# Optimization experiments

Hardware: AMD Instinct MI355X
Metric: run time of the kernel (lower is better)

The kernel has to match this reference:

```python
import jax, jax.numpy as jnp
import numpy as np


def _cdist_p2(x, y):
    # x: [N, t1, h], y: [N, t2, h] -> [N, t1, t2] Euclidean distances
    x2 = jnp.sum(x * x, axis=-1)  # [N, t1]
    y2 = jnp.sum(y * y, axis=-1)  # [N, t2]
    xy = jnp.einsum('nik,njk->nij', x, y)  # [N, t1, t2]
    d2 = x2[:, :, None] + y2[None if False else slice(None), None, :] - 2.0 * xy
    d2 = jnp.maximum(d2, 0.0)
    return jnp.sqrt(d2)


def _solve_relaxed_wmd(scores, axis):
    # argmin + one-hot scatter + (mask*scores).mean() == sum of per-slice minima / scores.size
    idx = jnp.argmin(scores, axis=axis, keepdims=True)
    mins = jnp.take_along_axis(scores, idx, axis=axis)
    return jnp.sum(mins) / scores.size


def setup_inputs() -> dict:
    key = jax.random.key(0)
    kx, ky = jax.random.split(key)
    L, B, t1, t2, h = 4, 16, 1024, 1024, 128
    x = jax.random.normal(kx, (L, B, t1, h), dtype=jnp.float32)
    y = jax.random.normal(ky, (L, B, t2, h), dtype=jnp.float32)
    return {"x": x, "y": y}


def reference(x, y):
    L, B, t1, h = x.shape
    t2 = y.shape[2]
    xf = x.reshape(L * B, t1, h).astype(jnp.float32)
    yf = y.reshape(L * B, t2, h).astype(jnp.float32)
    scores = _cdist_p2(xf, yf)  # [L*B, t1, t2]
    forward_scores = _solve_relaxed_wmd(scores, axis=1)
    backward_scores = _solve_relaxed_wmd(scores, axis=2)
    return jnp.maximum(forward_scores, backward_scores)
```

## Files before the change

### kernel.cpp

```cpp
#include <hip/hip_runtime.h>

#define NB 64
#define T 1024
#define HD 128

#define EINF 0xFF800000u

typedef __attribute__((ext_vector_type(8))) short bf16x8;
typedef __attribute__((ext_vector_type(4))) float f32x4;

static __device__ __forceinline__ short f2bf(float f) {
    unsigned u = __float_as_uint(f);
    u += 0x7FFFu + ((u >> 16) & 1u);
    return (short)(u >> 16);
}

static __device__ __forceinline__ unsigned fenc(float f) {
    unsigned b = __float_as_uint(f);
    return b ^ (unsigned)(((int)b >> 31) | (int)0x80000000);
}
static __device__ __forceinline__ float fdec(unsigned u) {
    unsigned m = (~(unsigned)((int)u >> 31)) | 0x80000000u;
    return __uint_as_float(u ^ m);
}

__global__ void wmd_init(unsigned* __restrict__ g_colmin, float* __restrict__ sums) {
    int t = blockIdx.x * 256 + threadIdx.x;
    if (t < NB * T) g_colmin[t] = EINF;
    if (t < 2) sums[t] = 0.f;
}

__global__ void wmd_convy(const float* __restrict__ y, short* __restrict__ ybf,
                          float* __restrict__ y2) {
    int idx = blockIdx.x * 256 + threadIdx.x;
    float4 v = reinterpret_cast<const float4*>(y)[idx];
    short4 s4;
    s4.x = f2bf(v.x); s4.y = f2bf(v.y); s4.z = f2bf(v.z); s4.w = f2bf(v.w);
    reinterpret_cast<short4*>(ybf)[idx] = s4;
    float p = v.x * v.x + v.y * v.y + v.z * v.z + v.w * v.w;
    p += __shfl_xor(p, 1);  p += __shfl_xor(p, 2);  p += __shfl_xor(p, 4);
    p += __shfl_xor(p, 8);  p += __shfl_xor(p, 16);
    if ((threadIdx.x & 31) == 0) y2[idx >> 5] = p;
}

__global__ __launch_bounds__(256, 2)
void wmd_main(const float* __restrict__ x, const short* __restrict__ ybf,
              const float* __restrict__ y2, unsigned* __restrict__ g_colmin,
              float* __restrict__ g_rowmin) {
    __shared__ short b_sm[2][128 * 128];
    __shared__ float x2_sm[128];
    __shared__ unsigned col_min_sm[1024];
    __shared__ unsigned row_min_sm[128];

    const int tid  = threadIdx.x;
    const int n    = blockIdx.y;
    const int i0   = blockIdx.x * 128;
    const int lane = tid & 63;
    const int wave = tid >> 6;
    const int wm   = wave >> 1, wn = wave & 1;
    const int l16  = lane & 15, quad = lane >> 4;
    const float FINF = __uint_as_float(0x7F800000u);

    #pragma unroll
    for (int e = tid; e < 1024; e += 256) col_min_sm[e] = EINF;
    if (tid < 128) row_min_sm[tid] = EINF;

    {
        const float4* xg = reinterpret_cast<const float4*>(x + (size_t)(n * T + i0) * HD);
        #pragma unroll
        for (int it = 0; it < 16; ++it) {
            int idx = it * 256 + tid;
            int row = idx >> 5, c4 = idx & 31;
            float4 v = xg[idx];
            short4 s4;
            s4.x = f2bf(v.x); s4.y = f2bf(v.y); s4.z = f2bf(v.z); s4.w = f2bf(v.w);
            int c  = c4 >> 1;
            int sw = c ^ (row & 7);
            *reinterpret_cast<short4*>(&b_sm[0][(row * 16 + sw) * 8 + (c4 & 1) * 4]) = s4;
            float p = v.x * v.x + v.y * v.y + v.z * v.z + v.w * v.w;
            p += __shfl_xor(p, 1);  p += __shfl_xor(p, 2);  p += __shfl_xor(p, 4);
            p += __shfl_xor(p, 8);  p += __shfl_xor(p, 16);
            if ((tid & 31) == 0) x2_sm[row] = p;
        }
    }
    __syncthreads();

    bf16x8 af[4][4];
    #pragma unroll
    for (int mi = 0; mi < 4; ++mi)
        #pragma unroll
        for (int kk = 0; kk < 4; ++kk) {
            int row = wm * 64 + mi * 16 + l16;
            int c   = kk * 4 + quad;
            af[mi][kk] = *reinterpret_cast<const bf16x8*>(
                &b_sm[0][(row * 16 + (c ^ (row & 7))) * 8]);
        }
    float x2v[16];
    #pragma unroll
    for (int mi = 0; mi < 4; ++mi)
        #pragma unroll
        for (int r = 0; r < 4; ++r)
            x2v[mi * 4 + r] = x2_sm[wm * 64 + mi * 16 + quad * 4 + r];
    float rmin[16];
    #pragma unroll
    for (int q = 0; q < 16; ++q) rmin[q] = FINF;

#define ISSUE_GLLS(pbuf, jtile)                                                   \
    {                                                                             \
        const short* ybase = ybf + (((size_t)(n * T + (jtile) * 128)) << 7);      \
        _Pragma("unroll")                                                         \
        for (int it = 0; it < 8; ++it) {                                          \
            int g   = wave * 8 + it;                                              \
            int s   = g * 64 + lane;                                              \
            int row = s >> 4;                                                     \
            int c   = (s & 15) ^ (row & 7);                                       \
            const short* gp = ybase + row * 128 + c * 8;                          \
            __builtin_amdgcn_global_load_lds(                                     \
                (const __attribute__((address_space(1))) void*)gp,                \
                (__attribute__((address_space(3))) void*)&b_sm[pbuf][g * 512],    \
                16, 0, 0);                                                        \
        }                                                                         \
    }

    ISSUE_GLLS(1, 0);

    for (int jt = 0; jt < 8; ++jt) {
        const int p = (jt & 1) ^ 1;
        __syncthreads();
        if (jt < 7) ISSUE_GLLS(p ^ 1, jt + 1);

        float y2v[4];
        #pragma unroll
        for (int ni = 0; ni < 4; ++ni)
            y2v[ni] = y2[n * T + jt * 128 + wn * 64 + ni * 16 + l16];

        f32x4 acc[4][4];
        #pragma unroll
        for (int mi = 0; mi < 4; ++mi)
            #pragma unroll
            for (int ni = 0; ni < 4; ++ni) {
                f32x4 z = {0.f, 0.f, 0.f, 0.f};
                acc[mi][ni] = z;
            }

        #pragma unroll
        for (int kk = 0; kk < 4; ++kk) {
            bf16x8 bv[4];
            #pragma unroll
            for (int ni = 0; ni < 4; ++ni) {
                int row = wn * 64 + ni * 16 + l16;
                int c   = kk * 4 + quad;
                bv[ni] = *reinterpret_cast<const bf16x8*>(
                    &b_sm[p][(row * 16 + (c ^ (row & 7))) * 8]);
            }
            #pragma unroll
            for (int mi = 0; mi < 4; ++mi)
                #pragma unroll
                for (int ni = 0; ni < 4; ++ni)
                    acc[mi][ni] = __builtin_amdgcn_mfma_f32_16x16x32_bf16(
                        af[mi][kk], bv[ni], acc[mi][ni], 0, 0, 0);
        }

        float vcol[4] = {FINF, FINF, FINF, FINF};
        #pragma unroll
        for (int mi = 0; mi < 4; ++mi)
            #pragma unroll
            for (int r = 0; r < 4; ++r) {
                float x2r = x2v[mi * 4 + r];
                #pragma unroll
                for (int ni = 0; ni < 4; ++ni) {
                    float xy = acc[mi][ni][r];
                    rmin[mi * 4 + r] = fminf(rmin[mi * 4 + r], fmaf(-2.f, xy, y2v[ni]));
                    vcol[ni]         = fminf(vcol[ni],         fmaf(-2.f, xy, x2r));
                }
            }
        #pragma unroll
        for (int ni = 0; ni < 4; ++ni) {
            float v = vcol[ni];
            v = fminf(v, __shfl_xor(v, 16));
            v = fminf(v, __shfl_xor(v, 32));
            if (lane < 16)
                atomicMin(&col_min_sm[jt * 128 + wn * 64 + ni * 16 + lane], fenc(v));
        }
    }

    #pragma unroll
    for (int mi = 0; mi < 4; ++mi)
        #pragma unroll
        for (int r = 0; r < 4; ++r) {
            float v = rmin[mi * 4 + r];
            v = fminf(v, __shfl_xor(v, 1));
            v = fminf(v, __shfl_xor(v, 2));
            v = fminf(v, __shfl_xor(v, 4));
            v = fminf(v, __shfl_xor(v, 8));
            if (l16 == 0)
                atomicMin(&row_min_sm[wm * 64 + mi * 16 + quad * 4 + r], fenc(v));
        }
    __syncthreads();
    if (tid < 128) {
        float rv = fdec(row_min_sm[tid]) + x2_sm[tid];
        g_rowmin[n * T + i0 + tid] = fmaxf(rv, 0.f);
    }
    #pragma unroll
    for (int e = tid; e < 1024; e += 256)
        atomicMin(&g_colmin[n * T + e], col_min_sm[e]);
}

__global__ void wmd_reduce(const unsigned* __restrict__ g_colmin,
                           const float* __restrict__ g_rowmin,
                           const float* __restrict__ y2,
                           float* __restrict__ sums) {
    int n = blockIdx.x, t = threadIdx.x;
    float sc = 0.f, sr = 0.f;
    for (int e = t; e < T; e += 256) {
        float cv = fdec(g_colmin[n * T + e]) + y2[n * T + e];
        sc += sqrtf(fmaxf(cv, 0.f));
        sr += sqrtf(g_rowmin[n * T + e]);
    }
    #pragma unroll
    for (int o = 1; o < 64; o <<= 1) {
        sc += __shfl_xor(sc, o);
        sr += __shfl_xor(sr, o);
    }
    __shared__ float bc[4], br[4];
    int lane = t & 63, wv = t >> 6;
    if (lane == 0) { bc[wv] = sc; br[wv] = sr; }
    __syncthreads();
    if (t == 0) {
        atomicAdd(&sums[0], bc[0] + bc[1] + bc[2] + bc[3]);
        atomicAdd(&sums[1], br[0] + br[1] + br[2] + br[3]);
    }
}

__global__ void wmd_finalize(const float* __restrict__ sums, float* __restrict__ out) {
    out[0] = fmaxf(sums[0], sums[1]) * (1.0f / 67108864.0f);
}

extern "C" void kernel_launch(void* const* d_in, const int* in_sizes, int n_in,
                              void* d_out, int out_size, void* d_ws, size_t ws_size,
                              hipStream_t stream) {
    const float* x = (const float*)d_in[0];
    const float* y = (const float*)d_in[1];
    float* out = (float*)d_out;

    char* ws = (char*)d_ws;
    unsigned* g_colmin = (unsigned*)(ws);
    float*    g_rowmin = (float*)(ws + 256 * 1024);
    float*    y2       = (float*)(ws + 512 * 1024);
    float*    sums     = (float*)(ws + 768 * 1024);
    short*    ybf      = (short*)(ws + 1024 * 1024);

    wmd_init<<<(NB * T + 255) / 256, 256, 0, stream>>>(g_colmin, sums);
    wmd_convy<<<(NB * T * HD / 4) / 256, 256, 0, stream>>>(y, ybf, y2);
    wmd_main<<<dim3(T / 128, NB), 256, 0, stream>>>(x, ybf, y2, g_colmin, g_rowmin);
    wmd_reduce<<<NB, 256, 0, stream>>>(g_colmin, g_rowmin, y2, sums);
    wmd_finalize<<<1, 1, 0, stream>>>(sums, out);
}
```

Before: 136.1 us.

## Split column range across blocks, shrink tiles, fuse init kernels and finalize

The main kernel now splits each batch's j range into two halves of 512, so the grid doubles to 16x64 blocks. Each block uses 64-row B tiles and one 32-row A slab per wave, which lowers LDS and register use enough to allow 4 blocks per CU. Row minima go to global memory through atomicMin, and x2 is written out so the reduce kernel can finish the row sums. Init is merged into the y-conversion kernel, and the finalize kernel is replaced by a last-block counter inside reduce, which removes two launches. In exchange, each x tile is loaded twice and there is more global atomic traffic.

```diff
diff --git a/kernel.cpp b/kernel.cpp
--- a/kernel.cpp
+++ b/kernel.cpp
@@ -14,7 +14,6 @@
     u += 0x7FFFu + ((u >> 16) & 1u);
     return (short)(u >> 16);
 }
-
 static __device__ __forceinline__ unsigned fenc(float f) {
     unsigned b = __float_as_uint(f);
     return b ^ (unsigned)(((int)b >> 31) | (int)0x80000000);
@@ -24,93 +23,52 @@
     return __uint_as_float(u ^ m);
 }
 
-__global__ void wmd_init(unsigned* __restrict__ g_colmin, float* __restrict__ sums) {
-    int t = blockIdx.x * 256 + threadIdx.x;
-    if (t < NB * T) g_colmin[t] = EINF;
-    if (t < 2) sums[t] = 0.f;
-}
-
-__global__ void wmd_convy(const float* __restrict__ y, short* __restrict__ ybf,
-                          float* __restrict__ y2) {
-    int idx = blockIdx.x * 256 + threadIdx.x;
-    float4 v = reinterpret_cast<const float4*>(y)[idx];
+__global__ void wmd_prep(const float* __restrict__ y, short* __restrict__ ybf,
+                         float* __restrict__ y2, unsigned* __restrict__ g_colmin,
+                         unsigned* __restrict__ g_rowmin, float* __restrict__ sums,
+                         unsigned* __restrict__ counter) {
+    int gi = blockIdx.x * 256 + threadIdx.x;
+    float4 v = reinterpret_cast<const float4*>(y)[gi];
     short4 s4;
     s4.x = f2bf(v.x); s4.y = f2bf(v.y); s4.z = f2bf(v.z); s4.w = f2bf(v.w);
-    reinterpret_cast<short4*>(ybf)[idx] = s4;
+    reinterpret_cast<short4*>(ybf)[gi] = s4;
     float p = v.x * v.x + v.y * v.y + v.z * v.z + v.w * v.w;
     p += __shfl_xor(p, 1);  p += __shfl_xor(p, 2);  p += __shfl_xor(p, 4);
     p += __shfl_xor(p, 8);  p += __shfl_xor(p, 16);
-    if ((threadIdx.x & 31) == 0) y2[idx >> 5] = p;
-}
-
-__global__ __launch_bounds__(256, 2)
+    if ((threadIdx.x & 31) == 0) y2[gi >> 5] = p;
+    if (gi < NB * T) { g_colmin[gi] = EINF; g_rowmin[gi] = EINF; }
+    if (gi < 2) sums[gi] = 0.f;
+    if (gi == 2) counter[0] = 0u;
+}
+
+__global__ __launch_bounds__(256, 4)
 void wmd_main(const float* __restrict__ x, const short* __restrict__ ybf,
-              const float* __restrict__ y2, unsigned* __restrict__ g_colmin,
-              float* __restrict__ g_rowmin) {
-    __shared__ short b_sm[2][128 * 128];
+              const float* __restrict__ y2g, unsigned* __restrict__ g_colmin,
+              unsigned* __restrict__ g_rowmin, float* __restrict__ x2g) {
+    __shared__ short b_sm[2][64 * 128];
+    __shared__ float y2_sm[512];
     __shared__ float x2_sm[128];
-    __shared__ unsigned col_min_sm[1024];
-    __shared__ unsigned row_min_sm[128];
+    __shared__ unsigned col_min_sm[512];
 
     const int tid  = threadIdx.x;
     const int n    = blockIdx.y;
-    const int i0   = blockIdx.x * 128;
+    const int bx   = blockIdx.x;
+    const int i0   = (bx & 7) * 128;
+    const int j0   = (bx >> 3) * 512;
     const int lane = tid & 63;
     const int wave = tid >> 6;
-    const int wm   = wave >> 1, wn = wave & 1;
     const int l16  = lane & 15, quad = lane >> 4;
     const float FINF = __uint_as_float(0x7F800000u);
 
     #pragma unroll
-    for (int e = tid; e < 1024; e += 256) col_min_sm[e] = EINF;
-    if (tid < 128) row_min_sm[tid] = EINF;
-
-    {
-        const float4* xg = reinterpret_cast<const float4*>(x + (size_t)(n * T + i0) * HD);
-        #pragma unroll
-        for (int it = 0; it < 16; ++it) {
-            int idx = it * 256 + tid;
-            int row = idx >> 5, c4 = idx & 31;
-            float4 v = xg[idx];
-            short4 s4;
-            s4.x = f2bf(v.x); s4.y = f2bf(v.y); s4.z = f2bf(v.z); s4.w = f2bf(v.w);
-            int c  = c4 >> 1;
-            int sw = c ^ (row & 7);
-            *reinterpret_cast<short4*>(&b_sm[0][(row * 16 + sw) * 8 + (c4 & 1) * 4]) = s4;
-            float p = v.x * v.x + v.y * v.y + v.z * v.z + v.w * v.w;
-            p += __shfl_xor(p, 1);  p += __shfl_xor(p, 2);  p += __shfl_xor(p, 4);
-            p += __shfl_xor(p, 8);  p += __shfl_xor(p, 16);
-            if ((tid & 31) == 0) x2_sm[row] = p;
-        }
-    }
-    __syncthreads();
-
-    bf16x8 af[4][4];
-    #pragma unroll
-    for (int mi = 0; mi < 4; ++mi)
-        #pragma unroll
-        for (int kk = 0; kk < 4; ++kk) {
-            int row = wm * 64 + mi * 16 + l16;
-            int c   = kk * 4 + quad;
-            af[mi][kk] = *reinterpret_cast<const bf16x8*>(
-                &b_sm[0][(row * 16 + (c ^ (row & 7))) * 8]);
-        }
-    float x2v[16];
-    #pragma unroll
-    for (int mi = 0; mi < 4; ++mi)
-        #pragma unroll
-        for (int r = 0; r < 4; ++r)
-            x2v[mi * 4 + r] = x2_sm[wm * 64 + mi * 16 + quad * 4 + r];
-    float rmin[16];
-    #pragma unroll
-    for (int q = 0; q < 16; ++q) rmin[q] = FINF;
+    for (int e = tid; e < 512; e += 256) col_min_sm[e] = EINF;
 
 #define ISSUE_GLLS(pbuf, jtile)                                                   \
     {                                                                             \
-        const short* ybase = ybf + (((size_t)(n * T + (jtile) * 128)) << 7);      \
+        const short* ybase = ybf + (((size_t)(n * T + j0 + (jtile) * 64)) << 7);  \
         _Pragma("unroll")                                                         \
-        for (int it = 0; it < 8; ++it) {                                          \
-            int g   = wave * 8 + it;                                              \
+        for (int it = 0; it < 4; ++it) {                                          \
+            int g   = wave * 4 + it;                                              \
             int s   = g * 64 + lane;                                              \
             int row = s >> 4;                                                     \
             int c   = (s & 15) ^ (row & 7);                                       \
@@ -122,21 +80,59 @@
         }                                                                         \
     }
 
-    ISSUE_GLLS(1, 0);
+    ISSUE_GLLS(0, 0);
+
+    bf16x8 af[2][4];
+    #pragma unroll
+    for (int mi = 0; mi < 2; ++mi) {
+        float part = 0.f;
+        #pragma unroll
+        for (int kk = 0; kk < 4; ++kk) {
+            const float4* gp = reinterpret_cast<const float4*>(
+                x + (((size_t)(n * T + i0 + wave * 32 + mi * 16 + l16)) << 7) + kk * 32 + quad * 8);
+            float4 a = gp[0], b = gp[1];
+            bf16x8 f;
+            f[0] = f2bf(a.x); f[1] = f2bf(a.y); f[2] = f2bf(a.z); f[3] = f2bf(a.w);
+            f[4] = f2bf(b.x); f[5] = f2bf(b.y); f[6] = f2bf(b.z); f[7] = f2bf(b.w);
+            af[mi][kk] = f;
+            part += a.x * a.x + a.y * a.y + a.z * a.z + a.w * a.w;
+            part += b.x * b.x + b.y * b.y + b.z * b.z + b.w * b.w;
+        }
+        part += __shfl_xor(part, 16);
+        part += __shfl_xor(part, 32);
+        if (quad == 0) {
+            x2_sm[wave * 32 + mi * 16 + l16] = part;
+            x2g[n * T + i0 + wave * 32 + mi * 16 + l16] = part;
+        }
+    }
+    #pragma unroll
+    for (int e = tid; e < 512; e += 256) y2_sm[e] = y2g[n * T + j0 + e];
+
+    float rmin[8];
+    #pragma unroll
+    for (int q = 0; q < 8; ++q) rmin[q] = FINF;
+
+    __syncthreads();
+
+    float x2v[8];
+    #pragma unroll
+    for (int mi = 0; mi < 2; ++mi)
+        #pragma unroll
+        for (int r = 0; r < 4; ++r)
+            x2v[mi * 4 + r] = x2_sm[wave * 32 + mi * 16 + quad * 4 + r];
 
     for (int jt = 0; jt < 8; ++jt) {
-        const int p = (jt & 1) ^ 1;
-        __syncthreads();
+        const int p = jt & 1;
         if (jt < 7) ISSUE_GLLS(p ^ 1, jt + 1);
 
         float y2v[4];
         #pragma unroll
         for (int ni = 0; ni < 4; ++ni)
-            y2v[ni] = y2[n * T + jt * 128 + wn * 64 + ni * 16 + l16];
-
-        f32x4 acc[4][4];
-        #pragma unroll
-        for (int mi = 0; mi < 4; ++mi)
+            y2v[ni] = y2_sm[jt * 64 + ni * 16 + l16];
+
+        f32x4 acc[2][4];
+        #pragma unroll
+        for (int mi = 0; mi < 2; ++mi)
             #pragma unroll
             for (int ni = 0; ni < 4; ++ni) {
                 f32x4 z = {0.f, 0.f, 0.f, 0.f};
@@ -148,13 +144,12 @@
             bf16x8 bv[4];
             #pragma unroll
             for (int ni = 0; ni < 4; ++ni) {
-                int row = wn * 64 + ni * 16 + l16;
-                int c   = kk * 4 + quad;
-                bv[ni] = *reinterpret_cast<const bf16x8*>(
-                    &b_sm[p][(row * 16 + (c ^ (row & 7))) * 8]);
+                int row = ni * 16 + l16;
+                int c   = (kk * 4 + quad) ^ (row & 7);
+                bv[ni] = *reinterpret_cast<const bf16x8*>(&b_sm[p][(row * 16 + c) * 8]);
             }
             #pragma unroll
-            for (int mi = 0; mi < 4; ++mi)
+            for (int mi = 0; mi < 2; ++mi)
                 #pragma unroll
                 for (int ni = 0; ni < 4; ++ni)
                     acc[mi][ni] = __builtin_amdgcn_mfma_f32_16x16x32_bf16(
@@ -163,7 +158,7 @@
 
         float vcol[4] = {FINF, FINF, FINF, FINF};
         #pragma unroll
-        for (int mi = 0; mi < 4; ++mi)
+        for (int mi = 0; mi < 2; ++mi)
             #pragma unroll
             for (int r = 0; r < 4; ++r) {
                 float x2r = x2v[mi * 4 + r];
@@ -180,12 +175,13 @@
             v = fminf(v, __shfl_xor(v, 16));
             v = fminf(v, __shfl_xor(v, 32));
             if (lane < 16)
-                atomicMin(&col_min_sm[jt * 128 + wn * 64 + ni * 16 + lane], fenc(v));
-        }
-    }
-
-    #pragma unroll
-    for (int mi = 0; mi < 4; ++mi)
+                atomicMin(&col_min_sm[jt * 64 + ni * 16 + lane], fenc(v));
+        }
+        __syncthreads();
+    }
+
+    #pragma unroll
+    for (int mi = 0; mi < 2; ++mi)
         #pragma unroll
         for (int r = 0; r < 4; ++r) {
             float v = rmin[mi * 4 + r];
@@ -194,28 +190,27 @@
             v = fminf(v, __shfl_xor(v, 4));
             v = fminf(v, __shfl_xor(v, 8));
             if (l16 == 0)
-                atomicMin(&row_min_sm[wm * 64 + mi * 16 + quad * 4 + r], fenc(v));
-        }
-    __syncthreads();
-    if (tid < 128) {
-        float rv = fdec(row_min_sm[tid]) + x2_sm[tid];
-        g_rowmin[n * T + i0 + tid] = fmaxf(rv, 0.f);
-    }
-    #pragma unroll
-    for (int e = tid; e < 1024; e += 256)
-        atomicMin(&g_colmin[n * T + e], col_min_sm[e]);
+                atomicMin(&g_rowmin[n * T + i0 + wave * 32 + mi * 16 + quad * 4 + r], fenc(v));
+        }
+    #pragma unroll
+    for (int e = tid; e < 512; e += 256)
+        atomicMin(&g_colmin[n * T + j0 + e], col_min_sm[e]);
 }
 
 __global__ void wmd_reduce(const unsigned* __restrict__ g_colmin,
-                           const float* __restrict__ g_rowmin,
-                           const float* __restrict__ y2,
-                           float* __restrict__ sums) {
+                           const unsigned* __restrict__ g_rowmin,
+                           const float* __restrict__ x2g,
+                           const float* __restrict__ y2g,
+                           float* __restrict__ sums,
+                           unsigned* __restrict__ counter,
+                           float* __restrict__ out) {
     int n = blockIdx.x, t = threadIdx.x;
     float sc = 0.f, sr = 0.f;
     for (int e = t; e < T; e += 256) {
-        float cv = fdec(g_colmin[n * T + e]) + y2[n * T + e];
+        float cv = fdec(g_colmin[n * T + e]) + y2g[n * T + e];
+        float rv = fdec(g_rowmin[n * T + e]) + x2g[n * T + e];
         sc += sqrtf(fmaxf(cv, 0.f));
-        sr += sqrtf(g_rowmin[n * T + e]);
+        sr += sqrtf(fmaxf(rv, 0.f));
     }
     #pragma unroll
     for (int o = 1; o < 64; o <<= 1) {
@@ -229,11 +224,14 @@
     if (t == 0) {
         atomicAdd(&sums[0], bc[0] + bc[1] + bc[2] + bc[3]);
         atomicAdd(&sums[1], br[0] + br[1] + br[2] + br[3]);
-    }
-}
-
-__global__ void wmd_finalize(const float* __restrict__ sums, float* __restrict__ out) {
-    out[0] = fmaxf(sums[0], sums[1]) * (1.0f / 67108864.0f);
+        __threadfence();
+        unsigned old = atomicAdd(counter, 1u);
+        if (old == NB - 1) {
+            float a = atomicAdd(&sums[0], 0.f);
+            float b = atomicAdd(&sums[1], 0.f);
+            out[0] = fmaxf(a, b) * (1.0f / 67108864.0f);
+        }
+    }
 }
 
 extern "C" void kernel_launch(void* const* d_in, const int* in_sizes, int n_in,
@@ -245,14 +243,15 @@
 
     char* ws = (char*)d_ws;
     unsigned* g_colmin = (unsigned*)(ws);
-    float*    g_rowmin = (float*)(ws + 256 * 1024);
-    float*    y2       = (float*)(ws + 512 * 1024);
-    float*    sums     = (float*)(ws + 768 * 1024);
-    short*    ybf      = (short*)(ws + 1024 * 1024);
-
-    wmd_init<<<(NB * T + 255) / 256, 256, 0, stream>>>(g_colmin, sums);
-    wmd_convy<<<(NB * T * HD / 4) / 256, 256, 0, stream>>>(y, ybf, y2);
-    wmd_main<<<dim3(T / 128, NB), 256, 0, stream>>>(x, ybf, y2, g_colmin, g_rowmin);
-    wmd_reduce<<<NB, 256, 0, stream>>>(g_colmin, g_rowmin, y2, sums);
-    wmd_finalize<<<1, 1, 0, stream>>>(sums, out);
-}
+    unsigned* g_rowmin = (unsigned*)(ws + 256 * 1024);
+    float*    x2g      = (float*)(ws + 512 * 1024);
+    float*    y2g      = (float*)(ws + 768 * 1024);
+    float*    sums     = (float*)(ws + 1024 * 1024);
+    unsigned* counter  = (unsigned*)(ws + 1024 * 1024 + 8);
+    short*    ybf      = (short*)(ws + 1024 * 1024 + 4096);
+
+    wmd_prep<<<(NB * T * HD / 4) / 256, 256, 0, stream>>>(y, ybf, y2g, g_colmin,
+                                                          g_rowmin, sums, counter);
+    wmd_main<<<dim3(16, NB), 256, 0, stream>>>(x, ybf, y2g, g_colmin, g_rowmin, x2g);
+    wmd_reduce<<<NB, 256, 0, stream>>>(g_colmin, g_rowmin, x2g, y2g, sums, counter, out);
+}
```

Result: faster. 127.4 us (-6.4%).
